# Kernel tuning notes

Measured on AMD Instinct MI355X. Metric: run time of the kernel, lower is better.

Reference implementation:

```python
import jax, jax.numpy as jnp
import numpy as np

N = 131072   # total utterances (nodes)
B = 2048     # conversations (segments)
F = 200      # n_features (hard-coded 200 in source)
STEPS = 3    # processing_steps (reason_steps[0])


def setup_inputs() -> dict:
    key = jax.random.key(0)
    k = jax.random.split(key, 8)
    x = jax.random.normal(k[0], (N, F), dtype=jnp.float32)
    batch = jnp.sort(jax.random.randint(k[1], (N,), 0, B, dtype=jnp.int32))
    cos_coef = jax.random.normal(k[2], (N,), dtype=jnp.float32)
    q_star = jax.random.normal(k[3], (B, 2 * F), dtype=jnp.float32)
    s = 1.0 / np.sqrt(F)
    # PyTorch LSTM params: gate order i, f, g, o; input size 2F, hidden F
    W_ih = jax.random.uniform(k[4], (4 * F, 2 * F), jnp.float32, -s, s)
    W_hh = jax.random.uniform(k[5], (4 * F, F), jnp.float32, -s, s)
    b_ih = jax.random.uniform(k[6], (4 * F,), jnp.float32, -s, s)
    b_hh = jax.random.uniform(k[7], (4 * F,), jnp.float32, -s, s)
    return {"x": x, "batch": batch, "cos_coef": cos_coef, "q_star": q_star,
            "W_ih": W_ih, "W_hh": W_hh, "b_ih": b_ih, "b_hh": b_hh}


def _lstm_cell(inp, h, c, W_ih, W_hh, b_ih, b_hh):
    gates = inp @ W_ih.T + b_ih + h @ W_hh.T + b_hh  # [B, 4F]
    i, f, g, o = jnp.split(gates, 4, axis=-1)
    c = jax.nn.sigmoid(f) * c + jax.nn.sigmoid(i) * jnp.tanh(g)
    h = jax.nn.sigmoid(o) * jnp.tanh(c)
    return h, c


def reference(x, batch, cos_coef, q_star, W_ih, W_hh, b_ih, b_hh):
    # initial LSTM hidden: a_sit[i] = cos_row_i @ x[segment_i]  -> segment_sum
    h = jax.ops.segment_sum(cos_coef[:, None] * x, batch, num_segments=B)  # [B,F]
    c = jnp.zeros((B, F), dtype=x.dtype)
    for _ in range(STEPS):
        h, c = _lstm_cell(q_star, h, c, W_ih, W_hh, b_ih, b_hh)
        q = h                                            # [B,F]
        e = jnp.sum(x * q[batch], axis=-1)               # [N]
        m = jax.ops.segment_max(e, batch, num_segments=B)
        ex = jnp.exp(e - m[batch])
        denom = jax.ops.segment_sum(ex, batch, num_segments=B)
        a = ex / denom[batch]                            # per-segment softmax
        r = jax.ops.segment_sum(a[:, None] * x, batch, num_segments=B)  # [B,F]
        q_star = jnp.concatenate([q, r], axis=-1)        # [B,2F]
    return q_star
```

## Files before the change

kernel.cpp:

```cpp
#include <hip/hip_runtime.h>
#include <hip/hip_bf16.h>

#define N_NODES 131072
#define B_SEG   2048
#define F_DIM   200
#define K_DIM   608
#define NEG_INF (-3.4e38f)

typedef __attribute__((ext_vector_type(8))) short bf16x8;
typedef __attribute__((ext_vector_type(4))) float f32x4;

__device__ __forceinline__ float b2f(unsigned short u) {
  union { unsigned int i; float f; } v; v.i = ((unsigned int)u) << 16; return v.f;
}
__device__ __forceinline__ unsigned short f2bu(float f) {
  __hip_bfloat16 h = __float2bfloat16(f);
  return *reinterpret_cast<unsigned short*>(&h);
}
__device__ __forceinline__ float sigmoidf_(float x) { return 1.f / (1.f + __expf(-x)); }
__device__ __forceinline__ int lower_bound(const int* __restrict__ a, int n, int v) {
  int lo = 0, hi = n;
  while (lo < hi) { int mid = (lo + hi) >> 1; if (a[mid] < v) lo = mid + 1; else hi = mid; }
  return lo;
}

__global__ __launch_bounds__(256) void init_setup_kernel(
    const float* __restrict__ xf, const int* __restrict__ batch,
    const float* __restrict__ cosc, const float* __restrict__ qs0,
    const float* __restrict__ Wih, const float* __restrict__ Whh,
    const float* __restrict__ bih, const float* __restrict__ bhh,
    unsigned short* __restrict__ xb, unsigned short* __restrict__ A,
    unsigned short* __restrict__ Wc, float* __restrict__ bsum,
    int* __restrict__ seg_off) {
  int bid = blockIdx.x, tid = threadIdx.x;
  if (bid >= 2048) {
    if (bid < 4024) {
      int idx = (bid - 2048) * 256 + tid;
      int row = idx / K_DIM, k = idx - row * K_DIM;
      float v = 0.f;
      if (row < 800) {
        if (k < 400)      v = Wih[row * 400 + k];
        else if (k < 600) v = Whh[row * 200 + (k - 400)];
      }
      Wc[idx] = f2bu(v);
    } else if (bid < 4536) {
      int i = (bid - 4024) * 256 + tid;
      int v  = batch[i];
      int pv = (i == 0) ? -1 : batch[i - 1];
      for (int b = pv + 1; b <= v; b++) seg_off[b] = i;
    } else {
      int idx = (bid - 4536) * 256 + tid;
      if (idx < 800) bsum[idx] = bih[idx] + bhh[idx];
      else if (idx == 800) {
        int last = batch[N_NODES - 1];
        for (int b = last + 1; b <= B_SEG; b++) seg_off[b] = N_NODES;
      }
    }
    return;
  }
  __shared__ float rpart[5][F_DIM];
  int b = bid;
  int start = lower_bound(batch, N_NODES, b);
  int end   = lower_bound(batch, N_NODES, b + 1);
  int n = end - start;
  unsigned short* Arow = A + (size_t)b * K_DIM;
  int rgrp = tid / 50, col4 = tid - rgrp * 50;
  float a0 = 0.f, a1 = 0.f, a2 = 0.f, a3 = 0.f;
  if (rgrp < 5) {
    int r = rgrp;
    float4 vc; float cc = 0.f;
    if (r < n) {
      vc = *(const float4*)(xf + (size_t)(start + r) * F_DIM + 4 * col4);
      cc = cosc[start + r];
    }
    while (r < n) {
      int rn = r + 5;
      float4 vn; float cn2 = 0.f;
      if (rn < n) {
        vn = *(const float4*)(xf + (size_t)(start + rn) * F_DIM + 4 * col4);
        cn2 = cosc[start + rn];
      }
      ushort4 o; o.x = f2bu(vc.x); o.y = f2bu(vc.y); o.z = f2bu(vc.z); o.w = f2bu(vc.w);
      *(ushort4*)(xb + (size_t)(start + r) * F_DIM + 4 * col4) = o;
      a0 += cc * b2f(o.x); a1 += cc * b2f(o.y);
      a2 += cc * b2f(o.z); a3 += cc * b2f(o.w);
      vc = vn; cc = cn2; r = rn;
    }
    rpart[rgrp][4 * col4]     = a0;
    rpart[rgrp][4 * col4 + 1] = a1;
    rpart[rgrp][4 * col4 + 2] = a2;
    rpart[rgrp][4 * col4 + 3] = a3;
  }
  if (tid < 100) {
    float4 v = *(const float4*)(qs0 + (size_t)b * 400 + 4 * tid);
    ushort4 o; o.x = f2bu(v.x); o.y = f2bu(v.y); o.z = f2bu(v.z); o.w = f2bu(v.w);
    *(ushort4*)(Arow + 4 * tid) = o;
  }
  if (tid < 8) Arow[600 + tid] = 0;
  __syncthreads();
  if (tid < F_DIM) {
    float acc = rpart[0][tid] + rpart[1][tid] + rpart[2][tid] + rpart[3][tid]
              + rpart[4][tid];
    Arow[400 + tid] = f2bu(acc);
  }
}

__global__ __launch_bounds__(256) void gemm_gates(
    const unsigned short* __restrict__ A, const unsigned short* __restrict__ W,
    float* __restrict__ gates) {
  int tid = threadIdx.x;
  int bm = blockIdx.x * 32, bn = blockIdx.y * 64;
  int wave = tid >> 6, lane = tid & 63;
  int quad = lane >> 4, col = lane & 15;
  int strip = wave >> 1;
  int tp = (wave & 1) * 2;
  f32x4 acc[2];
  acc[0] = (f32x4){0.f, 0.f, 0.f, 0.f};
  acc[1] = (f32x4){0.f, 0.f, 0.f, 0.f};
  const unsigned short* Ap = A + (size_t)(bm + strip * 16 + col) * K_DIM + quad * 8;
  const unsigned short* Wp = W + (size_t)(bn + col) * K_DIM + quad * 8;
#pragma unroll
  for (int k0 = 0; k0 < K_DIM; k0 += 32) {
    bf16x8 af = *(const bf16x8*)(Ap + k0);
#pragma unroll
    for (int t = 0; t < 2; t++) {
      bf16x8 bfr = *(const bf16x8*)(Wp + (size_t)(tp + t) * 16 * K_DIM + k0);
      acc[t] = __builtin_amdgcn_mfma_f32_16x16x32_bf16(af, bfr, acc[t], 0, 0, 0);
    }
  }
#pragma unroll
  for (int t = 0; t < 2; t++) {
    int gn = bn + (tp + t) * 16 + col;
    if (gn < 800) {
#pragma unroll
      for (int r = 0; r < 4; r++) {
        int gm = bm + strip * 16 + quad * 4 + r;
        gates[(size_t)gm * 800 + gn] = acc[t][r];
      }
    }
  }
}

__global__ __launch_bounds__(256) void attn_fused(
    const unsigned short* __restrict__ xb, const int* __restrict__ seg_off,
    const float* __restrict__ gates, const float* __restrict__ bsum,
    float* __restrict__ cvec, unsigned short* __restrict__ A,
    float* __restrict__ out, int step) {
  __shared__ float q_s[F_DIM];
  __shared__ float rpart[8][F_DIM];
  __shared__ float redm[8], redl[8];
  int b = blockIdx.x, tid = threadIdx.x;
  int start = seg_off[b], end = seg_off[b + 1];
  int n = end - start;
  unsigned short* Arow = A + (size_t)b * K_DIM;
  if (tid < F_DIM) {
    int f = tid;
    const float* g = gates + (size_t)b * 800;
    float gi = g[f]       + bsum[f];
    float gf = g[200 + f] + bsum[200 + f];
    float gg = g[400 + f] + bsum[400 + f];
    float go = g[600 + f] + bsum[600 + f];
    float cp = (step > 0) ? cvec[(size_t)b * F_DIM + f] : 0.f;
    float cn = sigmoidf_(gf) * cp + sigmoidf_(gi) * tanhf(gg);
    float hn = sigmoidf_(go) * tanhf(cn);
    cvec[(size_t)b * F_DIM + f] = cn;
    q_s[f] = hn;
    if (step < 2) {
      unsigned short hb = f2bu(hn);
      Arow[f] = hb;
      Arow[400 + f] = hb;
    }
  }
  __syncthreads();
  int wave = tid >> 6, lane = tid & 63;
  int half = lane >> 5, hl = lane & 31;
  int hw = wave * 2 + half;
  bool act = (hl < 25);
  float q0=0,q1=0,q2=0,q3=0,q4=0,q5=0,q6=0,q7=0;
  if (act) {
    q0 = q_s[8*hl];   q1 = q_s[8*hl+1]; q2 = q_s[8*hl+2]; q3 = q_s[8*hl+3];
    q4 = q_s[8*hl+4]; q5 = q_s[8*hl+5]; q6 = q_s[8*hl+6]; q7 = q_s[8*hl+7];
  }
  const unsigned short* xp = xb + (size_t)start * F_DIM + 8 * hl;
  float m = NEG_INF, l = 0.f;
  float a0=0,a1=0,a2=0,a3=0,a4=0,a5=0,a6=0,a7=0;
  int r = hw;
  uint4 vc = (uint4){0,0,0,0};
  if (act && r < n) vc = *(const uint4*)(xp + (size_t)r * F_DIM);
  while (r < n) {
    int rn = r + 8;
    uint4 vn = (uint4){0,0,0,0};
    if (act && rn < n) vn = *(const uint4*)(xp + (size_t)rn * F_DIM);
    float x0=0,x1=0,x2=0,x3=0,x4=0,x5=0,x6=0,x7=0;
    float p = 0.f;
    if (act) {
      x0 = b2f((unsigned short)(vc.x & 0xffff)); x1 = b2f((unsigned short)(vc.x >> 16));
      x2 = b2f((unsigned short)(vc.y & 0xffff)); x3 = b2f((unsigned short)(vc.y >> 16));
      x4 = b2f((unsigned short)(vc.z & 0xffff)); x5 = b2f((unsigned short)(vc.z >> 16));
      x6 = b2f((unsigned short)(vc.w & 0xffff)); x7 = b2f((unsigned short)(vc.w >> 16));
      p = q0*x0 + q1*x1 + q2*x2 + q3*x3 + q4*x4 + q5*x5 + q6*x6 + q7*x7;
    }
#pragma unroll
    for (int off = 16; off; off >>= 1) p += __shfl_xor(p, off, 32);
    float e = p;
    float mn = fmaxf(m, e);
    float fac = __expf(m - mn);
    float w  = __expf(e - mn);
    l  = l * fac + w;
    a0 = a0*fac + w*x0; a1 = a1*fac + w*x1; a2 = a2*fac + w*x2; a3 = a3*fac + w*x3;
    a4 = a4*fac + w*x4; a5 = a5*fac + w*x5; a6 = a6*fac + w*x6; a7 = a7*fac + w*x7;
    m = mn;
    vc = vn; r = rn;
  }
  if (hl == 0) redm[hw] = m;
  __syncthreads();
  float M = fmaxf(fmaxf(fmaxf(redm[0], redm[1]), fmaxf(redm[2], redm[3])),
                  fmaxf(fmaxf(redm[4], redm[5]), fmaxf(redm[6], redm[7])));
  float facw = (m > NEG_INF) ? __expf(m - M) : 0.f;
  if (hl == 0) redl[hw] = l * facw;
  if (act) {
    float* rp = &rpart[hw][8 * hl];
    rp[0] = a0*facw; rp[1] = a1*facw; rp[2] = a2*facw; rp[3] = a3*facw;
    rp[4] = a4*facw; rp[5] = a5*facw; rp[6] = a6*facw; rp[7] = a7*facw;
  }
  __syncthreads();
  float L = redl[0]+redl[1]+redl[2]+redl[3]+redl[4]+redl[5]+redl[6]+redl[7];
  float inv = (L > 0.f) ? 1.f / L : 0.f;
  if (tid < F_DIM) {
    float rv = (rpart[0][tid]+rpart[1][tid]+rpart[2][tid]+rpart[3][tid]
              + rpart[4][tid]+rpart[5][tid]+rpart[6][tid]+rpart[7][tid]) * inv;
    if (step < 2) {
      Arow[200 + tid] = f2bu(rv);
    } else {
      out[(size_t)b * 400 + tid]       = q_s[tid];
      out[(size_t)b * 400 + 200 + tid] = rv;
    }
  }
}

extern "C" void kernel_launch(void* const* d_in, const int* in_sizes, int n_in,
                              void* d_out, int out_size, void* d_ws, size_t ws_size,
                              hipStream_t stream) {
  const float* x    = (const float*)d_in[0];
  const int*   batch= (const int*)d_in[1];
  const float* cosc = (const float*)d_in[2];
  const float* qs0  = (const float*)d_in[3];
  const float* Wih  = (const float*)d_in[4];
  const float* Whh  = (const float*)d_in[5];
  const float* bih  = (const float*)d_in[6];
  const float* bhh  = (const float*)d_in[7];
  char* ws = (char*)d_ws;
  unsigned short* xb   = (unsigned short*)(ws);
  unsigned short* A    = (unsigned short*)(ws + 52428800);
  unsigned short* Wc   = (unsigned short*)(ws + 54919168);
  float*          gates= (float*)(ws + 55930880);
  float*          cvec = (float*)(ws + 62484480);
  float*          bsum = (float*)(ws + 64122880);
  int*            soff = (int*)(ws + 64126080);
  float*          outp = (float*)d_out;

  init_setup_kernel<<<4540, 256, 0, stream>>>(x, batch, cosc, qs0, Wih, Whh,
                                              bih, bhh, xb, A, Wc, bsum, soff);
  for (int s = 0; s < 3; s++) {
    gemm_gates<<<dim3(64, 13), 256, 0, stream>>>(A, Wc, gates);
    attn_fused<<<B_SEG, 256, 0, stream>>>(xb, soff, gates, bsum, cvec, A, outp, s);
  }
}
```

Measured before the change: 279.1 us.

## Split x bf16 conversion into flat streaming kernel and separate h0 segment-sum kernel

Moves the fp32-to-bf16 conversion of x out of the per-segment init blocks into a flat, fully coalesced streaming pass where each thread handles eight float4 elements. A new h0 kernel then computes the cosine-weighted segment sum from the bf16 copy, using the precomputed segment offsets instead of binary searches and eight row groups instead of five. The aim is to replace the uneven, segment-bound conversion with a bandwidth-friendly stream. The cost is an extra launch and an extra read of the bf16 x.

New measurement: 277.3 us. Within noise of the previous version (-0.6%).

```diff
diff --git a/kernel.cpp b/kernel.cpp
--- a/kernel.cpp
+++ b/kernel.cpp
@@ -6,6 +6,8 @@
 #define F_DIM   200
 #define K_DIM   608
 #define NEG_INF (-3.4e38f)
+#define CONV_B  3200
+#define CONV_T  (CONV_B * 256)
 
 typedef __attribute__((ext_vector_type(8))) short bf16x8;
 typedef __attribute__((ext_vector_type(4))) float f32x4;
@@ -18,89 +20,99 @@
   return *reinterpret_cast<unsigned short*>(&h);
 }
 __device__ __forceinline__ float sigmoidf_(float x) { return 1.f / (1.f + __expf(-x)); }
-__device__ __forceinline__ int lower_bound(const int* __restrict__ a, int n, int v) {
-  int lo = 0, hi = n;
-  while (lo < hi) { int mid = (lo + hi) >> 1; if (a[mid] < v) lo = mid + 1; else hi = mid; }
-  return lo;
-}
-
-__global__ __launch_bounds__(256) void init_setup_kernel(
+
+__global__ __launch_bounds__(256) void convert_setup_kernel(
     const float* __restrict__ xf, const int* __restrict__ batch,
-    const float* __restrict__ cosc, const float* __restrict__ qs0,
     const float* __restrict__ Wih, const float* __restrict__ Whh,
     const float* __restrict__ bih, const float* __restrict__ bhh,
-    unsigned short* __restrict__ xb, unsigned short* __restrict__ A,
-    unsigned short* __restrict__ Wc, float* __restrict__ bsum,
-    int* __restrict__ seg_off) {
+    unsigned short* __restrict__ xb, unsigned short* __restrict__ Wc,
+    float* __restrict__ bsum, int* __restrict__ seg_off) {
   int bid = blockIdx.x, tid = threadIdx.x;
-  if (bid >= 2048) {
-    if (bid < 4024) {
-      int idx = (bid - 2048) * 256 + tid;
-      int row = idx / K_DIM, k = idx - row * K_DIM;
-      float v = 0.f;
-      if (row < 800) {
-        if (k < 400)      v = Wih[row * 400 + k];
-        else if (k < 600) v = Whh[row * 200 + (k - 400)];
-      }
-      Wc[idx] = f2bu(v);
-    } else if (bid < 4536) {
-      int i = (bid - 4024) * 256 + tid;
-      int v  = batch[i];
-      int pv = (i == 0) ? -1 : batch[i - 1];
-      for (int b = pv + 1; b <= v; b++) seg_off[b] = i;
-    } else {
-      int idx = (bid - 4536) * 256 + tid;
-      if (idx < 800) bsum[idx] = bih[idx] + bhh[idx];
-      else if (idx == 800) {
-        int last = batch[N_NODES - 1];
-        for (int b = last + 1; b <= B_SEG; b++) seg_off[b] = N_NODES;
-      }
-    }
-    return;
-  }
-  __shared__ float rpart[5][F_DIM];
-  int b = bid;
-  int start = lower_bound(batch, N_NODES, b);
-  int end   = lower_bound(batch, N_NODES, b + 1);
+  if (bid < CONV_B) {
+    int t = bid * 256 + tid;
+    const float4* src = (const float4*)xf;
+    ushort4* dst = (ushort4*)xb;
+    float4 v[8];
+#pragma unroll
+    for (int j = 0; j < 8; j++) v[j] = src[t + j * CONV_T];
+#pragma unroll
+    for (int j = 0; j < 8; j++) {
+      ushort4 o; o.x = f2bu(v[j].x); o.y = f2bu(v[j].y);
+      o.z = f2bu(v[j].z); o.w = f2bu(v[j].w);
+      dst[t + j * CONV_T] = o;
+    }
+  } else if (bid < CONV_B + 1976) {
+    int idx = (bid - CONV_B) * 256 + tid;
+    int row = idx / K_DIM, k = idx - row * K_DIM;
+    float v = 0.f;
+    if (row < 800) {
+      if (k < 400)      v = Wih[row * 400 + k];
+      else if (k < 600) v = Whh[row * 200 + (k - 400)];
+    }
+    Wc[idx] = f2bu(v);
+  } else if (bid < CONV_B + 1976 + 512) {
+    int i = (bid - CONV_B - 1976) * 256 + tid;
+    int v  = batch[i];
+    int pv = (i == 0) ? -1 : batch[i - 1];
+    for (int b = pv + 1; b <= v; b++) seg_off[b] = i;
+  } else {
+    int idx = (bid - CONV_B - 2488) * 256 + tid;
+    if (idx < 800) bsum[idx] = bih[idx] + bhh[idx];
+    else if (idx == 800) {
+      int last = batch[N_NODES - 1];
+      for (int b = last + 1; b <= B_SEG; b++) seg_off[b] = N_NODES;
+    }
+  }
+}
+
+__global__ __launch_bounds__(256) void h0_kernel(
+    const unsigned short* __restrict__ xb, const int* __restrict__ seg_off,
+    const float* __restrict__ cosc, const float* __restrict__ qs0,
+    unsigned short* __restrict__ A) {
+  __shared__ float rpart[8][F_DIM];
+  int b = blockIdx.x, tid = threadIdx.x;
+  int start = seg_off[b], end = seg_off[b + 1];
   int n = end - start;
   unsigned short* Arow = A + (size_t)b * K_DIM;
-  int rgrp = tid / 50, col4 = tid - rgrp * 50;
-  float a0 = 0.f, a1 = 0.f, a2 = 0.f, a3 = 0.f;
-  if (rgrp < 5) {
-    int r = rgrp;
-    float4 vc; float cc = 0.f;
-    if (r < n) {
-      vc = *(const float4*)(xf + (size_t)(start + r) * F_DIM + 4 * col4);
-      cc = cosc[start + r];
-    }
-    while (r < n) {
-      int rn = r + 5;
-      float4 vn; float cn2 = 0.f;
-      if (rn < n) {
-        vn = *(const float4*)(xf + (size_t)(start + rn) * F_DIM + 4 * col4);
-        cn2 = cosc[start + rn];
-      }
-      ushort4 o; o.x = f2bu(vc.x); o.y = f2bu(vc.y); o.z = f2bu(vc.z); o.w = f2bu(vc.w);
-      *(ushort4*)(xb + (size_t)(start + r) * F_DIM + 4 * col4) = o;
-      a0 += cc * b2f(o.x); a1 += cc * b2f(o.y);
-      a2 += cc * b2f(o.z); a3 += cc * b2f(o.w);
-      vc = vn; cc = cn2; r = rn;
-    }
-    rpart[rgrp][4 * col4]     = a0;
-    rpart[rgrp][4 * col4 + 1] = a1;
-    rpart[rgrp][4 * col4 + 2] = a2;
-    rpart[rgrp][4 * col4 + 3] = a3;
-  }
   if (tid < 100) {
     float4 v = *(const float4*)(qs0 + (size_t)b * 400 + 4 * tid);
     ushort4 o; o.x = f2bu(v.x); o.y = f2bu(v.y); o.z = f2bu(v.z); o.w = f2bu(v.w);
     *(ushort4*)(Arow + 4 * tid) = o;
   }
   if (tid < 8) Arow[600 + tid] = 0;
+  int wave = tid >> 6, lane = tid & 63;
+  int half = lane >> 5, hl = lane & 31;
+  int hw = wave * 2 + half;
+  bool act = (hl < 25);
+  const unsigned short* xp = xb + (size_t)start * F_DIM + 8 * hl;
+  float a0=0,a1=0,a2=0,a3=0,a4=0,a5=0,a6=0,a7=0;
+  int r = hw;
+  uint4 vc = (uint4){0,0,0,0}; float cc = 0.f;
+  if (r < n) { if (act) vc = *(const uint4*)(xp + (size_t)r * F_DIM); cc = cosc[start + r]; }
+  while (r < n) {
+    int rn = r + 8;
+    uint4 vn = (uint4){0,0,0,0}; float cn2 = 0.f;
+    if (rn < n) { if (act) vn = *(const uint4*)(xp + (size_t)rn * F_DIM); cn2 = cosc[start + rn]; }
+    if (act) {
+      a0 += cc * b2f((unsigned short)(vc.x & 0xffff));
+      a1 += cc * b2f((unsigned short)(vc.x >> 16));
+      a2 += cc * b2f((unsigned short)(vc.y & 0xffff));
+      a3 += cc * b2f((unsigned short)(vc.y >> 16));
+      a4 += cc * b2f((unsigned short)(vc.z & 0xffff));
+      a5 += cc * b2f((unsigned short)(vc.z >> 16));
+      a6 += cc * b2f((unsigned short)(vc.w & 0xffff));
+      a7 += cc * b2f((unsigned short)(vc.w >> 16));
+    }
+    vc = vn; cc = cn2; r = rn;
+  }
+  if (act) {
+    float* rp = &rpart[hw][8 * hl];
+    rp[0]=a0; rp[1]=a1; rp[2]=a2; rp[3]=a3; rp[4]=a4; rp[5]=a5; rp[6]=a6; rp[7]=a7;
+  }
   __syncthreads();
   if (tid < F_DIM) {
-    float acc = rpart[0][tid] + rpart[1][tid] + rpart[2][tid] + rpart[3][tid]
-              + rpart[4][tid];
+    float acc = rpart[0][tid]+rpart[1][tid]+rpart[2][tid]+rpart[3][tid]
+              + rpart[4][tid]+rpart[5][tid]+rpart[6][tid]+rpart[7][tid];
     Arow[400 + tid] = f2bu(acc);
   }
 }
@@ -259,8 +271,9 @@
   int*            soff = (int*)(ws + 64126080);
   float*          outp = (float*)d_out;
 
-  init_setup_kernel<<<4540, 256, 0, stream>>>(x, batch, cosc, qs0, Wih, Whh,
-                                              bih, bhh, xb, A, Wc, bsum, soff);
+  convert_setup_kernel<<<CONV_B + 1976 + 512 + 4, 256, 0, stream>>>(
+      x, batch, Wih, Whh, bih, bhh, xb, Wc, bsum, soff);
+  h0_kernel<<<B_SEG, 256, 0, stream>>>(xb, soff, cosc, qs0, A);
   for (int s = 0; s < 3; s++) {
     gemm_gates<<<dim3(64, 13), 256, 0, stream>>>(A, Wc, gates);
     attn_fused<<<B_SEG, 256, 0, stream>>>(xb, soff, gates, bsum, cvec, A, outp, s);
```
